# Kernel optimization log

Hardware: AMD Instinct MI355X
Metric: run time of the kernel (lower is better)

The kernel has to match this reference:

```python
import jax, jax.numpy as jnp
import numpy as np
import math

L = 16
F = 2
T = 2 ** 19  # hashmap size (power of two)
BASE_RES = 16
MAX_RES = 2048
GROWTH = math.exp((math.log(MAX_RES) - math.log(BASE_RES)) / (L - 1))
RESOLUTIONS = np.array([int(math.ceil(BASE_RES * GROWTH ** l)) for l in range(L)], dtype=np.float32)
PRIMES = np.array([1, 2654435761, 805459861], dtype=np.uint32)
# 8 corner offsets of a unit cube, ordered as in the torch module
OFFSETS = np.array([[0,0,0],[0,0,1],[0,1,0],[0,1,1],[1,0,0],[1,0,1],[1,1,0],[1,1,1]], dtype=np.int32)
BBOX_MIN, BBOX_MAX = -1.0, 1.0


def setup_inputs() -> dict:
    key = jax.random.key(0)
    k1, k2 = jax.random.split(key)
    N = 1_000_000
    # world-space positions uniformly inside the default bbox [-1, 1]^3
    positions = jax.random.uniform(k1, (N, 3), dtype=jnp.float32, minval=-1.0, maxval=1.0)
    # hash tables init: uniform(-1e-4, 1e-4), matching nn.init.uniform_
    hash_tables = jax.random.uniform(k2, (L, T, F), dtype=jnp.float32, minval=-1e-4, maxval=1e-4)
    return {"positions": positions, "hash_tables": hash_tables}


def _hash_grid_forward(positions, hash_tables):
    res = jnp.asarray(RESOLUTIONS)                      # [L]
    primes = jnp.asarray(PRIMES)                        # [3] uint32
    offsets = jnp.asarray(OFFSETS)                      # [8,3] int32

    normalized = (positions - BBOX_MIN) / (BBOX_MAX - BBOX_MIN + 1e-8)
    normalized = jnp.clip(normalized, 0.0, 1.0 - 1e-6)  # [N,3]
    scaled = normalized[:, None, :] * res[None, :, None]  # [N,L,3]
    floor_coords = jnp.floor(scaled).astype(jnp.int32)
    frac = scaled - floor_coords.astype(jnp.float32)      # [N,L,3]

    corners = floor_coords[:, :, None, :] + offsets[None, None, :, :]  # [N,L,8,3]
    # spatial hash: (x*p0 ^ y*p1 ^ z*p2) mod T; uint32 wrap-around is
    # equivalent to the int64 torch version modulo T since T | 2^32
    c = corners.astype(jnp.uint32)
    h = (c[..., 0] * primes[0]) ^ (c[..., 1] * primes[1]) ^ (c[..., 2] * primes[2])
    hash_idx = (h % jnp.uint32(T)).astype(jnp.int32)      # [N,L,8]

    level_off = (jnp.arange(L, dtype=jnp.int32) * T)[None, :, None]  # [1,L,1]
    flat_idx = level_off + hash_idx                        # [N,L,8]
    corner_feats = hash_tables.reshape(L * T, F)[flat_idx]  # [N,L,8,F]

    fx = frac[..., 0:1]  # [N,L,1]
    fy = frac[..., 1:2]
    fz = frac[..., 2:3]
    c00 = corner_feats[:, :, 0] * (1 - fz) + corner_feats[:, :, 1] * fz
    c01 = corner_feats[:, :, 2] * (1 - fz) + corner_feats[:, :, 3] * fz
    c10 = corner_feats[:, :, 4] * (1 - fz) + corner_feats[:, :, 5] * fz
    c11 = corner_feats[:, :, 6] * (1 - fz) + corner_feats[:, :, 7] * fz
    c0 = c00 * (1 - fy) + c01 * fy
    c1 = c10 * (1 - fy) + c11 * fy
    out = c0 * (1 - fx) + c1 * fx                          # [N,L,F]
    return out.reshape(positions.shape[0], L * F)


def reference(positions, hash_tables):
    return _hash_grid_forward(positions, hash_tables)
```

## Files before the change

### kernel.cpp

```cpp
#include <hip/hip_runtime.h>
#include <math.h>

#define NUM_LEVELS 16
#define T_SIZE (1u << 19)
#define T_MASK (T_SIZE - 1u)
#define PRIME1 2654435761u
#define PRIME2 805459861u

struct ResParams { float r[NUM_LEVELS]; };

typedef float f32x2 __attribute__((ext_vector_type(2)));
typedef float f32x4 __attribute__((ext_vector_type(4)));

__device__ __forceinline__ void nt_store_f2(float2 v, float2* p) {
    f32x2 x; x.x = v.x; x.y = v.y;
    __builtin_nontemporal_store(x, (f32x2*)p);
}
__device__ __forceinline__ float2 nt_load_f2(const float2* p) {
    f32x2 x = __builtin_nontemporal_load((const f32x2*)p);
    float2 r; r.x = x.x; r.y = x.y; return r;
}
__device__ __forceinline__ void nt_store_f4(f32x4 v, float* p) {
    __builtin_nontemporal_store(v, (f32x4*)p);
}

struct CornerSet {
    unsigned idx[8];
    unsigned ux;
    float fx, fy, fz;
};

__device__ __forceinline__ void calc_corners(
    float px, float py, float pz, float res, unsigned base, CornerSet& cs)
{
    float nx = (px + 1.0f) * 0.5f;
    float ny = (py + 1.0f) * 0.5f;
    float nz = (pz + 1.0f) * 0.5f;
    const float HI = 0.999999f;
    nx = fminf(fmaxf(nx, 0.0f), HI);
    ny = fminf(fmaxf(ny, 0.0f), HI);
    nz = fminf(fmaxf(nz, 0.0f), HI);

    float sx = nx * res, sy = ny * res, sz = nz * res;
    float flx = floorf(sx), fly = floorf(sy), flz = floorf(sz);
    cs.fx = sx - flx; cs.fy = sy - fly; cs.fz = sz - flz;

    unsigned ux = (unsigned)(int)flx;
    unsigned uy = (unsigned)(int)fly;
    unsigned uz = (unsigned)(int)flz;
    cs.ux = ux;

    unsigned hx0 = ux;            unsigned hx1 = ux + 1u;
    unsigned hy0 = uy * PRIME1;   unsigned hy1 = hy0 + PRIME1;
    unsigned hz0 = uz * PRIME2;   unsigned hz1 = hz0 + PRIME2;

    cs.idx[0] = base + ((hx0 ^ hy0 ^ hz0) & T_MASK);
    cs.idx[1] = base + ((hx0 ^ hy0 ^ hz1) & T_MASK);
    cs.idx[2] = base + ((hx0 ^ hy1 ^ hz0) & T_MASK);
    cs.idx[3] = base + ((hx0 ^ hy1 ^ hz1) & T_MASK);
    cs.idx[4] = base + ((hx1 ^ hy0 ^ hz0) & T_MASK);
    cs.idx[5] = base + ((hx1 ^ hy0 ^ hz1) & T_MASK);
    cs.idx[6] = base + ((hx1 ^ hy1 ^ hz0) & T_MASK);
    cs.idx[7] = base + ((hx1 ^ hy1 ^ hz1) & T_MASK);
}

__device__ __forceinline__ void load_feats(
    const float2* __restrict__ table, const CornerSet& cs, float2 f[8])
{
    if ((cs.ux & 1u) == 0u) {
        const f32x4* t4 = reinterpret_cast<const f32x4*>(table);
#pragma unroll
        for (int j = 0; j < 4; ++j) {
            unsigned i0 = cs.idx[j];
            f32x4 v = t4[i0 >> 1];
            float2 lo; lo.x = v.x; lo.y = v.y;
            float2 hi; hi.x = v.z; hi.y = v.w;
            bool sw = (i0 & 1u) != 0u;
            f[j]     = sw ? hi : lo;
            f[4 + j] = sw ? lo : hi;
        }
    } else {
#pragma unroll
        for (int i = 0; i < 8; ++i) f[i] = table[cs.idx[i]];
    }
}

__device__ __forceinline__ float2 trilerp(const float2 f[8], float fx, float fy, float fz)
{
    float omz = 1.0f - fz, omy = 1.0f - fy, omx = 1.0f - fx;
    float c00x = f[0].x * omz + f[1].x * fz;
    float c00y = f[0].y * omz + f[1].y * fz;
    float c01x = f[2].x * omz + f[3].x * fz;
    float c01y = f[2].y * omz + f[3].y * fz;
    float c10x = f[4].x * omz + f[5].x * fz;
    float c10y = f[4].y * omz + f[5].y * fz;
    float c11x = f[6].x * omz + f[7].x * fz;
    float c11y = f[6].y * omz + f[7].y * fz;
    float c0x = c00x * omy + c01x * fy;
    float c0y = c00y * omy + c01y * fy;
    float c1x = c10x * omy + c11x * fy;
    float c1y = c10y * omy + c11y * fy;
    float2 o;
    o.x = c0x * omx + c1x * fx;
    o.y = c0y * omx + c1y * fx;
    return o;
}

__global__ __launch_bounds__(256) void hashgrid_gather_kernel(
    const float* __restrict__ pos,
    const float2* __restrict__ table,
    float2* __restrict__ ws,
    ResParams rp, int N)
{
    int level = blockIdx.y;
    int t = threadIdx.x;
    int n0 = blockIdx.x * 512 + 2 * t;
    int n1 = n0 + 1;
    bool v0 = n0 < N;
    bool v1 = n1 < N;
    if (!v0) return;

    float res = rp.r[level];
    unsigned base = (unsigned)level * T_SIZE;

    float px0 = pos[3 * n0 + 0], py0 = pos[3 * n0 + 1], pz0 = pos[3 * n0 + 2];
    int m1 = v1 ? n1 : n0;
    float px1 = pos[3 * m1 + 0], py1 = pos[3 * m1 + 1], pz1 = pos[3 * m1 + 2];

    CornerSet c0, c1;
    calc_corners(px0, py0, pz0, res, base, c0);
    calc_corners(px1, py1, pz1, res, base, c1);

    float2 f0[8], f1[8];
    load_feats(table, c0, f0);
    load_feats(table, c1, f1);

    float2 o0 = trilerp(f0, c0.fx, c0.fy, c0.fz);
    float2 o1 = trilerp(f1, c1.fx, c1.fy, c1.fz);

    size_t w = (size_t)level * N + n0;
    if (v1) {
        f32x4 v; v.x = o0.x; v.y = o0.y; v.z = o1.x; v.w = o1.y;
        nt_store_f4(v, (float*)&ws[w]);
    } else {
        nt_store_f2(o0, &ws[w]);
    }
}

__global__ __launch_bounds__(256) void hashgrid_untile_kernel(
    const float2* __restrict__ ws,
    float* __restrict__ out,
    int N)
{
    int g = blockIdx.x * 256 + threadIdx.x;
    int p = g >> 3;
    int m = g & 7;
    if (p >= N) return;
    float2 a = nt_load_f2(&ws[(size_t)(2 * m) * N + p]);
    float2 b = nt_load_f2(&ws[(size_t)(2 * m + 1) * N + p]);
    f32x4 v; v.x = a.x; v.y = a.y; v.z = b.x; v.w = b.y;
    nt_store_f4(v, &out[(size_t)p * 32 + m * 4]);
}

__global__ __launch_bounds__(256) void hashgrid_fused_kernel(
    const float* __restrict__ pos,
    const float2* __restrict__ table,
    float2* __restrict__ out,
    ResParams rp, int N)
{
    int tid = blockIdx.x * blockDim.x + threadIdx.x;
    int n = tid >> 4;
    int l = tid & 15;
    if (n >= N) return;
    float px = pos[3 * n + 0], py = pos[3 * n + 1], pz = pos[3 * n + 2];
    CornerSet c;
    calc_corners(px, py, pz, rp.r[l], (unsigned)l * T_SIZE, c);
    float2 f[8];
    load_feats(table, c, f);
    out[tid] = trilerp(f, c.fx, c.fy, c.fz);
}

extern "C" void kernel_launch(void* const* d_in, const int* in_sizes, int n_in,
                              void* d_out, int out_size, void* d_ws, size_t ws_size,
                              hipStream_t stream) {
    const float*  pos   = (const float*)d_in[0];
    const float2* table = (const float2*)d_in[1];
    int N = in_sizes[0] / 3;

    ResParams rp;
    double growth = exp((log(2048.0) - log(16.0)) / 15.0);
    for (int l = 0; l < NUM_LEVELS; ++l) {
        rp.r[l] = (float)ceil(16.0 * pow(growth, (double)l));
    }

    size_t ws_needed = (size_t)NUM_LEVELS * (size_t)N * sizeof(float2);
    if (ws_size >= ws_needed) {
        float2* ws = (float2*)d_ws;
        int chunks = (N + 511) / 512;
        dim3 grid(chunks, NUM_LEVELS);
        hashgrid_gather_kernel<<<grid, 256, 0, stream>>>(pos, table, ws, rp, N);
        long long tthreads = (long long)N * 8;
        int tblocks = (int)((tthreads + 255) / 256);
        hashgrid_untile_kernel<<<tblocks, 256, 0, stream>>>(ws, (float*)d_out, N);
    } else {
        long long total = (long long)N * NUM_LEVELS;
        int grid = (int)((total + 255) / 256);
        hashgrid_fused_kernel<<<grid, 256, 0, stream>>>(pos, table, (float2*)d_out, rp, N);
    }
}
```

Measured before the change: 564.2 us.

## Fuse gather and untile into one per-point kernel looping over level pairs

Replaces the level-major gather kernel, its workspace, and the transpose kernel with a single kernel. Each thread owns one point, loops over all 16 levels two at a time, and writes its 32 outputs directly. This removes the 128MB workspace write and read and one launch. In exchange, the threads of a wave now hit all levels of the table, which hurts cache locality of the hash-table gathers. Each thread also carries a serial loop of eight iterations, and the 128-byte per-thread row stride leaves the output stores uncoalesced.

```diff
diff --git a/kernel.cpp b/kernel.cpp
--- a/kernel.cpp
+++ b/kernel.cpp
@@ -12,35 +12,15 @@
 typedef float f32x2 __attribute__((ext_vector_type(2)));
 typedef float f32x4 __attribute__((ext_vector_type(4)));
 
-__device__ __forceinline__ void nt_store_f2(float2 v, float2* p) {
-    f32x2 x; x.x = v.x; x.y = v.y;
-    __builtin_nontemporal_store(x, (f32x2*)p);
-}
-__device__ __forceinline__ float2 nt_load_f2(const float2* p) {
-    f32x2 x = __builtin_nontemporal_load((const f32x2*)p);
-    float2 r; r.x = x.x; r.y = x.y; return r;
-}
-__device__ __forceinline__ void nt_store_f4(f32x4 v, float* p) {
-    __builtin_nontemporal_store(v, (f32x4*)p);
-}
-
 struct CornerSet {
     unsigned idx[8];
     unsigned ux;
     float fx, fy, fz;
 };
 
-__device__ __forceinline__ void calc_corners(
-    float px, float py, float pz, float res, unsigned base, CornerSet& cs)
+__device__ __forceinline__ void calc_corners_n(
+    float nx, float ny, float nz, float res, unsigned base, CornerSet& cs)
 {
-    float nx = (px + 1.0f) * 0.5f;
-    float ny = (py + 1.0f) * 0.5f;
-    float nz = (pz + 1.0f) * 0.5f;
-    const float HI = 0.999999f;
-    nx = fminf(fmaxf(nx, 0.0f), HI);
-    ny = fminf(fmaxf(ny, 0.0f), HI);
-    nz = fminf(fmaxf(nz, 0.0f), HI);
-
     float sx = nx * res, sy = ny * res, sz = nz * res;
     float flx = floorf(sx), fly = floorf(sy), flz = floorf(sz);
     cs.fx = sx - flx; cs.fy = sy - fly; cs.fz = sz - flz;
@@ -106,78 +86,43 @@
     return o;
 }
 
-__global__ __launch_bounds__(256) void hashgrid_gather_kernel(
+__global__ __launch_bounds__(256) void hashgrid_fused16_kernel(
     const float* __restrict__ pos,
     const float2* __restrict__ table,
-    float2* __restrict__ ws,
+    float* __restrict__ out,
     ResParams rp, int N)
 {
-    int level = blockIdx.y;
-    int t = threadIdx.x;
-    int n0 = blockIdx.x * 512 + 2 * t;
-    int n1 = n0 + 1;
-    bool v0 = n0 < N;
-    bool v1 = n1 < N;
-    if (!v0) return;
+    int n = blockIdx.x * 256 + threadIdx.x;
+    if (n >= N) return;
 
-    float res = rp.r[level];
-    unsigned base = (unsigned)level * T_SIZE;
+    float px = pos[3 * n + 0], py = pos[3 * n + 1], pz = pos[3 * n + 2];
 
-    float px0 = pos[3 * n0 + 0], py0 = pos[3 * n0 + 1], pz0 = pos[3 * n0 + 2];
-    int m1 = v1 ? n1 : n0;
-    float px1 = pos[3 * m1 + 0], py1 = pos[3 * m1 + 1], pz1 = pos[3 * m1 + 2];
+    const float HI = 0.999999f;
+    float nx = fminf(fmaxf((px + 1.0f) * 0.5f, 0.0f), HI);
+    float ny = fminf(fmaxf((py + 1.0f) * 0.5f, 0.0f), HI);
+    float nz = fminf(fmaxf((pz + 1.0f) * 0.5f, 0.0f), HI);
 
-    CornerSet c0, c1;
-    calc_corners(px0, py0, pz0, res, base, c0);
-    calc_corners(px1, py1, pz1, res, base, c1);
+    float* po = out + (size_t)n * 32;
 
-    float2 f0[8], f1[8];
-    load_feats(table, c0, f0);
-    load_feats(table, c1, f1);
+#pragma unroll 1
+    for (int pr = 0; pr < 8; ++pr) {
+        int l0 = 2 * pr;
+        int l1 = 2 * pr + 1;
 
-    float2 o0 = trilerp(f0, c0.fx, c0.fy, c0.fz);
-    float2 o1 = trilerp(f1, c1.fx, c1.fy, c1.fz);
+        CornerSet c0, c1;
+        calc_corners_n(nx, ny, nz, rp.r[l0], (unsigned)l0 * T_SIZE, c0);
+        calc_corners_n(nx, ny, nz, rp.r[l1], (unsigned)l1 * T_SIZE, c1);
 
-    size_t w = (size_t)level * N + n0;
-    if (v1) {
+        float2 f0[8], f1[8];
+        load_feats(table, c0, f0);
+        load_feats(table, c1, f1);
+
+        float2 o0 = trilerp(f0, c0.fx, c0.fy, c0.fz);
+        float2 o1 = trilerp(f1, c1.fx, c1.fy, c1.fz);
+
         f32x4 v; v.x = o0.x; v.y = o0.y; v.z = o1.x; v.w = o1.y;
-        nt_store_f4(v, (float*)&ws[w]);
-    } else {
-        nt_store_f2(o0, &ws[w]);
+        *reinterpret_cast<f32x4*>(po + 4 * pr) = v;
     }
-}
-
-__global__ __launch_bounds__(256) void hashgrid_untile_kernel(
-    const float2* __restrict__ ws,
-    float* __restrict__ out,
-    int N)
-{
-    int g = blockIdx.x * 256 + threadIdx.x;
-    int p = g >> 3;
-    int m = g & 7;
-    if (p >= N) return;
-    float2 a = nt_load_f2(&ws[(size_t)(2 * m) * N + p]);
-    float2 b = nt_load_f2(&ws[(size_t)(2 * m + 1) * N + p]);
-    f32x4 v; v.x = a.x; v.y = a.y; v.z = b.x; v.w = b.y;
-    nt_store_f4(v, &out[(size_t)p * 32 + m * 4]);
-}
-
-__global__ __launch_bounds__(256) void hashgrid_fused_kernel(
-    const float* __restrict__ pos,
-    const float2* __restrict__ table,
-    float2* __restrict__ out,
-    ResParams rp, int N)
-{
-    int tid = blockIdx.x * blockDim.x + threadIdx.x;
-    int n = tid >> 4;
-    int l = tid & 15;
-    if (n >= N) return;
-    float px = pos[3 * n + 0], py = pos[3 * n + 1], pz = pos[3 * n + 2];
-    CornerSet c;
-    calc_corners(px, py, pz, rp.r[l], (unsigned)l * T_SIZE, c);
-    float2 f[8];
-    load_feats(table, c, f);
-    out[tid] = trilerp(f, c.fx, c.fy, c.fz);
 }
 
 extern "C" void kernel_launch(void* const* d_in, const int* in_sizes, int n_in,
@@ -193,18 +138,7 @@
         rp.r[l] = (float)ceil(16.0 * pow(growth, (double)l));
     }
 
-    size_t ws_needed = (size_t)NUM_LEVELS * (size_t)N * sizeof(float2);
-    if (ws_size >= ws_needed) {
-        float2* ws = (float2*)d_ws;
-        int chunks = (N + 511) / 512;
-        dim3 grid(chunks, NUM_LEVELS);
-        hashgrid_gather_kernel<<<grid, 256, 0, stream>>>(pos, table, ws, rp, N);
-        long long tthreads = (long long)N * 8;
-        int tblocks = (int)((tthreads + 255) / 256);
-        hashgrid_untile_kernel<<<tblocks, 256, 0, stream>>>(ws, (float*)d_out, N);
-    } else {
-        long long total = (long long)N * NUM_LEVELS;
-        int grid = (int)((total + 255) / 256);
-        hashgrid_fused_kernel<<<grid, 256, 0, stream>>>(pos, table, (float2*)d_out, rp, N);
-    }
+    int blocks = (N + 255) / 256;
+    hashgrid_fused16_kernel<<<blocks, 256, 0, stream>>>(
+        pos, table, (float*)d_out, rp, N);
 }
```

Result: slower. 955.8 us (+69.4%).
